# Performance work log

Measured on AMD Instinct MI355X. Metric: run time of the kernel, lower is better.

Reference implementation:

```python
import jax, jax.numpy as jnp
import numpy as np

DIM = 1536      # model dim
NH = 12         # num heads
HD = 128        # head dim
F, H, W = 3, 26, 48   # video latent grid (frames, height, width)
S = F * H * W   # sequence length = 3744
B = 1
EPS = 1e-6
C2 = HD // 2    # 64 rotary pairs per head
SPLITS = [C2 - 2 * (C2 // 3), C2 // 3, C2 // 3]  # [22, 21, 21] for (f, h, w)


def _rope_angles():
    """Wan rope_params: concat of per-axis inverse-frequency angle tables, [1024, 64]."""
    def rp(dim):  # returns [1024, dim//2]
        inv = 1.0 / (10000.0 ** (np.arange(0, dim, 2, dtype=np.float64) / dim))
        return np.outer(np.arange(1024, dtype=np.float64), inv)
    a = np.concatenate([rp(HD - 4 * (HD // 6)), rp(2 * (HD // 6)), rp(2 * (HD // 6))], axis=1)
    return jnp.asarray(a, jnp.float32)


def setup_inputs() -> dict:
    key = jax.random.key(0)
    ks = jax.random.split(key, 9)
    std = DIM ** -0.5
    return {
        "x": jax.random.normal(ks[0], (B, S, DIM), jnp.float32),
        "wq": jax.random.normal(ks[1], (DIM, DIM), jnp.float32) * std,
        "bq": jnp.zeros((DIM,), jnp.float32),
        "wk": jax.random.normal(ks[2], (DIM, DIM), jnp.float32) * std,
        "bk": jnp.zeros((DIM,), jnp.float32),
        "wv": jax.random.normal(ks[3], (DIM, DIM), jnp.float32) * std,
        "bv": jnp.zeros((DIM,), jnp.float32),
        "wo": jax.random.normal(ks[4], (DIM, DIM), jnp.float32) * std,
        "bo": jnp.zeros((DIM,), jnp.float32),
        "gq": jnp.ones((DIM,), jnp.float32),   # WanRMSNorm weight for q
        "gk": jnp.ones((DIM,), jnp.float32),   # WanRMSNorm weight for k
        "freqs": _rope_angles(),                # [1024, 64] rotary angles
        "seq_lens": jnp.full((B,), S, jnp.int32),
    }


def _rmsnorm(y, g):
    return y * jax.lax.rsqrt(jnp.mean(jnp.square(y), axis=-1, keepdims=True) + EPS) * g


def _rope_grid(freqs):
    """Build per-position rotary angles [S, C2] from the 3D grid (F,H,W)."""
    af = freqs[:F, :SPLITS[0]]                       # [F, 22]
    ah = freqs[:H, SPLITS[0]:SPLITS[0] + SPLITS[1]]  # [H, 21]
    aw = freqs[:W, SPLITS[0] + SPLITS[1]:]           # [W, 21]
    ang = jnp.concatenate([
        jnp.broadcast_to(af[:, None, None, :], (F, H, W, SPLITS[0])),
        jnp.broadcast_to(ah[None, :, None, :], (F, H, W, SPLITS[1])),
        jnp.broadcast_to(aw[None, None, :, :], (F, H, W, SPLITS[2])),
    ], axis=-1)
    return ang.reshape(S, C2)


def _rope_apply(t, cos, sin):
    # t: [B, S, NH, HD]; pairs (even, odd) rotated by angle.
    tp = t.reshape(B, S, NH, C2, 2)
    xr, xi = tp[..., 0], tp[..., 1]
    yr = xr * cos - xi * sin
    yi = xr * sin + xi * cos
    return jnp.stack([yr, yi], axis=-1).reshape(B, S, NH, HD)


def reference(x, wq, bq, wk, bk, wv, bv, wo, bo, gq, gk, freqs, seq_lens):
    q = _rmsnorm(x @ wq.T + bq, gq).reshape(B, S, NH, HD)
    k = _rmsnorm(x @ wk.T + bk, gk).reshape(B, S, NH, HD)
    v = (x @ wv.T + bv).reshape(B, S, NH, HD)

    ang = _rope_grid(freqs)                    # [S, C2]
    cos = jnp.cos(ang)[None, :, None, :]       # [1, S, 1, C2]
    sin = jnp.sin(ang)[None, :, None, :]
    q = _rope_apply(q, cos, sin)
    k = _rope_apply(k, cos, sin)

    scale = HD ** -0.5
    scores = jnp.einsum('bqhd,bkhd->bhqk', q, k) * scale   # [B, NH, S, S]
    kmask = jnp.arange(S)[None, :] < seq_lens[:, None]     # [B, S]
    scores = jnp.where(kmask[:, None, None, :], scores, jnp.float32(-1e9))
    attn = jax.nn.softmax(scores, axis=-1)
    out = jnp.einsum('bhqk,bkhd->bqhd', attn, v).reshape(B, S, DIM)
    return out @ wo.T + bo
```

## Files before the change

### kernel.cpp

```cpp
#include <hip/hip_runtime.h>
#include <stdint.h>


#define DIM   1536
#define S_TOT 3744
#define NHEAD 12
#define HD    128
#define QT    59
#define NT    117

using short8 = __attribute__((ext_vector_type(8))) short;
using f32x4  = __attribute__((ext_vector_type(4))) float;
using f32x2  = __attribute__((ext_vector_type(2))) float;

__device__ __forceinline__ unsigned short f2bf(float f) {
  unsigned u = __builtin_bit_cast(unsigned, f);
  u += 0x7fffu + ((u >> 16) & 1u);
  return (unsigned short)(u >> 16);
}

__device__ __forceinline__ void gl_lds16(const void* g, void* l) {
  auto gp = (const __attribute__((address_space(1))) unsigned int*)g;
  auto lp = (__attribute__((address_space(3))) unsigned int*)(uintptr_t)l;
  __builtin_amdgcn_global_load_lds(gp, lp, 16, 0, 0);
}

#define NX4 (S_TOT * DIM / 4)
#define NW4 (DIM * DIM / 4)
__global__ __launch_bounds__(256) void cvt5_kernel(
    const float* __restrict__ x, const float* __restrict__ wq,
    const float* __restrict__ wk, const float* __restrict__ wv,
    const float* __restrict__ wo,
    unsigned short* __restrict__ xb, unsigned short* __restrict__ wqb,
    unsigned short* __restrict__ wkb, unsigned short* __restrict__ wvb,
    unsigned short* __restrict__ wob) {
  int gid = blockIdx.x * 256 + threadIdx.x;
  const float* src; unsigned short* dst; int off;
  if (gid < NX4)                { src = x;  dst = xb;  off = gid; }
  else if (gid < NX4 + NW4)     { src = wq; dst = wqb; off = gid - NX4; }
  else if (gid < NX4 + 2 * NW4) { src = wk; dst = wkb; off = gid - NX4 - NW4; }
  else if (gid < NX4 + 3 * NW4) { src = wv; dst = wvb; off = gid - NX4 - 2 * NW4; }
  else if (gid < NX4 + 4 * NW4) { src = wo; dst = wob; off = gid - NX4 - 3 * NW4; }
  else return;
  float4 v = ((const float4*)src)[off];
  ushort4 o;
  o.x = f2bf(v.x); o.y = f2bf(v.y); o.z = f2bf(v.z); o.w = f2bf(v.w);
  ((ushort4*)dst)[off] = o;
}

__device__ __forceinline__ void gemm_body(const unsigned short* __restrict__ A,
                                          const unsigned short* __restrict__ W,
                                          const float* __restrict__ bias,
                                          float* __restrict__ outF,
                                          unsigned short* __restrict__ outB,
                                          int M, int mode) {
  constexpr int K = DIM, N = DIM;
  __shared__ unsigned short As[128 * 32];
  __shared__ unsigned short Ws[128 * 32];
  int tid = threadIdx.x;
  int w = tid >> 6, lane = tid & 63;
  int wr = w >> 1, wc = w & 1, q4 = lane >> 4, ql = lane & 15;
  int m0 = blockIdx.y * 128, n0 = blockIdx.x * 128;

  f32x4 acc[4][4];
  const f32x4 zero4 = {0.f, 0.f, 0.f, 0.f};
#pragma unroll
  for (int i = 0; i < 4; i++)
#pragma unroll
    for (int j = 0; j < 4; j++) acc[i][j] = zero4;

  for (int k0 = 0; k0 < K; k0 += 32) {
    __syncthreads();
#pragma unroll
    for (int r = 0; r < 2; r++) {
      int idx = r * 256 + tid;
      int row = idx >> 2, ch = idx & 3;
      int am = m0 + row; am = (am < M) ? am : (M - 1);
      gl_lds16(A + (size_t)am * K + k0 + ch * 8, &As[idx * 8]);
      gl_lds16(W + (size_t)(n0 + row) * K + k0 + ch * 8, &Ws[idx * 8]);
    }
    __syncthreads();
    short8 af[4], wf[4];
#pragma unroll
    for (int i = 0; i < 4; i++)
      af[i] = *(const short8*)&As[(wr * 64 + i * 16 + ql) * 32 + q4 * 8];
#pragma unroll
    for (int j = 0; j < 4; j++)
      wf[j] = *(const short8*)&Ws[(wc * 64 + j * 16 + ql) * 32 + q4 * 8];
#pragma unroll
    for (int i = 0; i < 4; i++)
#pragma unroll
      for (int j = 0; j < 4; j++)
        acc[i][j] = __builtin_amdgcn_mfma_f32_16x16x32_bf16(af[i], wf[j], acc[i][j], 0, 0, 0);
  }

  float bb[4];
#pragma unroll
  for (int j = 0; j < 4; j++) bb[j] = bias[n0 + wc * 64 + j * 16 + ql];
#pragma unroll
  for (int i = 0; i < 4; i++) {
#pragma unroll
    for (int rg = 0; rg < 4; rg++) {
      int row = m0 + wr * 64 + i * 16 + q4 * 4 + rg;
      if (row < M) {
#pragma unroll
        for (int j = 0; j < 4; j++) {
          int col = n0 + wc * 64 + j * 16 + ql;
          float v = acc[i][j][rg] + bb[j];
          if (mode == 0) outF[(size_t)row * N + col] = v;
          else           outB[(size_t)row * N + col] = f2bf(v);
        }
      }
    }
  }
}

__global__ __launch_bounds__(256) void gemm_qkv_kernel(
    const unsigned short* __restrict__ xb,
    const unsigned short* __restrict__ wqb, const unsigned short* __restrict__ wkb,
    const unsigned short* __restrict__ wvb,
    const float* __restrict__ bq, const float* __restrict__ bk, const float* __restrict__ bv,
    float* __restrict__ Yq, float* __restrict__ Yk, unsigned short* __restrict__ Vb) {
  int z = blockIdx.z;
  const unsigned short* W = (z == 0) ? wqb : ((z == 1) ? wkb : wvb);
  const float* bias       = (z == 0) ? bq  : ((z == 1) ? bk  : bv);
  float* outF             = (z == 0) ? Yq  : Yk;
  gemm_body(xb, W, bias, outF, Vb, S_TOT, (z == 2) ? 1 : 0);
}

__global__ __launch_bounds__(256) void gemm_out_kernel(
    const unsigned short* __restrict__ AO, const unsigned short* __restrict__ wob,
    const float* __restrict__ bo, float* __restrict__ out) {
  gemm_body(AO, wob, bo, out, nullptr, S_TOT, 0);
}

__global__ __launch_bounds__(256) void normrope_kernel(
    const float* __restrict__ Yq, const float* __restrict__ Yk,
    const float* __restrict__ gq, const float* __restrict__ gk,
    const float* __restrict__ freqs,
    unsigned short* __restrict__ Qb, unsigned short* __restrict__ Kb) {
  int s = blockIdx.x;
  int tid = threadIdx.x;
  int w = tid >> 6, lane = tid & 63;
  const f32x2* yq2 = (const f32x2*)(Yq + (size_t)s * DIM);
  const f32x2* yk2 = (const f32x2*)(Yk + (size_t)s * DIM);
  f32x2 vq[3], vk[3];
  float ssq = 0.f, ssk = 0.f;
#pragma unroll
  for (int r = 0; r < 3; r++) {
    int p = tid + 256 * r;
    vq[r] = yq2[p]; vk[r] = yk2[p];
    ssq += vq[r].x * vq[r].x + vq[r].y * vq[r].y;
    ssk += vk[r].x * vk[r].x + vk[r].y * vk[r].y;
  }
#pragma unroll
  for (int d = 1; d < 64; d <<= 1) {
    ssq += __shfl_xor(ssq, d);
    ssk += __shfl_xor(ssk, d);
  }
  __shared__ float rq[4], rk[4];
  if (lane == 0) { rq[w] = ssq; rk[w] = ssk; }
  __syncthreads();
  float tq = rq[0] + rq[1] + rq[2] + rq[3];
  float tk = rk[0] + rk[1] + rk[2] + rk[3];
  const float SM_L2 = 0.08838834764831845f * 1.4426950408889634f;
  float invq = rsqrtf(tq * (1.f / DIM) + 1e-6f) * SM_L2;
  float invk = rsqrtf(tk * (1.f / DIM) + 1e-6f);

  int fi = s / (26 * 48);
  int hi = (s / 48) % 26;
  int wi = s % 48;
#pragma unroll
  for (int r = 0; r < 3; r++) {
    int p = tid + 256 * r;
    int c = p & 63;
    int frow = (c < 22) ? fi : ((c < 43) ? hi : wi);
    float ang = freqs[frow * 64 + c];
    float sn, cs;
    __sincosf(ang, &sn, &cs);
    {
      float a = vq[r].x * invq * gq[2 * p];
      float b = vq[r].y * invq * gq[2 * p + 1];
      ushort2 o; o.x = f2bf(a * cs - b * sn); o.y = f2bf(a * sn + b * cs);
      ((ushort2*)Qb)[(size_t)s * (DIM / 2) + p] = o;
    }
    {
      float a = vk[r].x * invk * gk[2 * p];
      float b = vk[r].y * invk * gk[2 * p + 1];
      ushort2 o; o.x = f2bf(a * cs - b * sn); o.y = f2bf(a * sn + b * cs);
      ((ushort2*)Kb)[(size_t)s * (DIM / 2) + p] = o;
    }
  }
}

__global__ __launch_bounds__(256) void vtrans_kernel(const unsigned short* __restrict__ Vb,
                                                     unsigned short* __restrict__ Vt) {
  int d0 = blockIdx.x * 64, s0 = blockIdx.y * 64;
  __shared__ unsigned short t[64][65];
  int tid = threadIdx.x;
#pragma unroll
  for (int r = 0; r < 4; r++) {
    int idx = r * 256 + tid;
    int sr = idx >> 4, c4 = (idx & 15) * 4;
    ushort4 v; v.x = v.y = v.z = v.w = 0;
    int s = s0 + sr;
    if (s < S_TOT) v = *(const ushort4*)(Vb + (size_t)s * DIM + d0 + c4);
    t[sr][c4 + 0] = v.x; t[sr][c4 + 1] = v.y; t[sr][c4 + 2] = v.z; t[sr][c4 + 3] = v.w;
  }
  __syncthreads();
#pragma unroll
  for (int r = 0; r < 4; r++) {
    int idx = r * 256 + tid;
    int dr = idx >> 4, s4 = (idx & 15) * 4;
    if (s0 + s4 < S_TOT) {
      ushort4 v;
      v.x = t[s4 + 0][dr]; v.y = t[s4 + 1][dr]; v.z = t[s4 + 2][dr]; v.w = t[s4 + 3][dr];
      *(ushort4*)(Vt + (size_t)(d0 + dr) * S_TOT + s0 + s4) = v;
    }
  }
}

__global__ __launch_bounds__(256, 3) void attn_kernel(
    const unsigned short* __restrict__ Qb, const unsigned short* __restrict__ Kb,
    const unsigned short* __restrict__ Vt, unsigned short* __restrict__ AO,
    const int* __restrict__ seq_lens) {
  const int NWG = QT * NHEAD;
  int bid = blockIdx.x;
  int xcd = bid & 7, bix = bid >> 3;
  const int qc = NWG >> 3, rr = NWG & 7;
  int wg = (xcd < rr ? xcd * (qc + 1) : rr * (qc + 1) + (xcd - rr) * qc) + bix;
  int h  = wg / QT;
  int qt = wg - h * QT;

  int tid = threadIdx.x;
  int w = tid >> 6, lane = tid & 63;
  int q4 = lane >> 4, ql = lane & 15;
  int seqlen = seq_lens[0]; if (seqlen > S_TOT) seqlen = S_TOT;

  __shared__ unsigned short Kl[2][32 * 128];
  __shared__ unsigned short Vl[2][128 * 32];
  __shared__ unsigned short Pl[4][16 * 40];

  int q0 = qt * 64 + w * 16;
  bool wact = (q0 < S_TOT);

  const size_t hoff = (size_t)h * HD;

  auto stage = [&](int buf, int t) {
    int k0 = t * 32;
    const unsigned short* kseg = Kb + (size_t)k0 * DIM + hoff;
#pragma unroll
    for (int r = 0; r < 2; r++) {
      int idx = r * 256 + tid;
      int row = idx >> 4, c = idx & 15;
      int g = c ^ (row & 15);
      gl_lds16(kseg + (size_t)row * DIM + g * 8, &Kl[buf][idx * 8]);
    }
#pragma unroll
    for (int r = 0; r < 2; r++) {
      int idx = r * 256 + tid;
      int row = idx >> 2, c = idx & 3;
      int g = c ^ (row & 3);
      gl_lds16(Vt + (hoff + row) * S_TOT + k0 + g * 8, &Vl[buf][idx * 8]);
    }
  };

  short8 qf[4];
  {
    int qrow = q0 + ql; if (qrow > S_TOT - 1) qrow = S_TOT - 1;
#pragma unroll
    for (int ks = 0; ks < 4; ks++)
      qf[ks] = *(const short8*)(Qb + (size_t)qrow * DIM + hoff + ks * 32 + q4 * 8);
  }
  asm volatile("s_waitcnt vmcnt(0)" ::: "memory");

  f32x4 o[8];
  const f32x4 zero4 = {0.f, 0.f, 0.f, 0.f};
#pragma unroll
  for (int nt = 0; nt < 8; nt++) o[nt] = zero4;
  float m_run = -3.0e38f, l_run = 0.f;

  stage(0, 0);

  for (int t = 0; t < NT; ++t) {
    int cur = t & 1;
    int k0 = t * 32;
    __builtin_amdgcn_s_barrier();
    asm volatile("" ::: "memory");
    if (t + 1 < NT) {
      stage(cur ^ 1, t + 1);
      asm volatile("s_waitcnt vmcnt(4)" ::: "memory");
    } else {
      asm volatile("s_waitcnt vmcnt(0)" ::: "memory");
    }
    __builtin_amdgcn_sched_barrier(0);
    __builtin_amdgcn_s_barrier();
    asm volatile("" ::: "memory");
    if (!wact) continue;

    f32x4 st[2];
    __builtin_amdgcn_s_setprio(1);
#pragma unroll
    for (int mt = 0; mt < 2; mt++) {
      st[mt] = zero4;
#pragma unroll
      for (int ks = 0; ks < 4; ks++) {
        int c = (ks * 4 + q4) ^ ql;
        short8 kf = *(const short8*)&Kl[cur][(mt * 16 + ql) * 128 + c * 8];
        st[mt] = __builtin_amdgcn_mfma_f32_16x16x32_bf16(kf, qf[ks], st[mt], 0, 0, 0);
      }
    }
    __builtin_amdgcn_s_setprio(0);

    float sc[8];
#pragma unroll
    for (int mt = 0; mt < 2; mt++)
#pragma unroll
      for (int rg = 0; rg < 4; rg++)
        sc[mt * 4 + rg] = st[mt][rg];
    if (k0 + 32 > seqlen) {
#pragma unroll
      for (int mt = 0; mt < 2; mt++)
#pragma unroll
        for (int rg = 0; rg < 4; rg++) {
          int key = k0 + mt * 16 + q4 * 4 + rg;
          if (key >= seqlen) sc[mt * 4 + rg] = -3.0e38f;
        }
    }
    float mloc = sc[0];
#pragma unroll
    for (int i = 1; i < 8; i++) mloc = fmaxf(mloc, sc[i]);
    mloc = fmaxf(mloc, __shfl_xor(mloc, 16));
    mloc = fmaxf(mloc, __shfl_xor(mloc, 32));

    if (!__all(mloc <= m_run + 8.0f)) {
      float mnew = fmaxf(m_run, mloc);
      float alpha = exp2f(m_run - mnew);
      m_run = mnew;
      l_run *= alpha;
      float ar[4];
#pragma unroll
      for (int rg = 0; rg < 4; rg++) ar[rg] = __shfl(alpha, q4 * 4 + rg, 16);
#pragma unroll
      for (int nt = 0; nt < 8; nt++)
#pragma unroll
        for (int rg = 0; rg < 4; rg++) o[nt][rg] *= ar[rg];
    }

    float lloc = 0.f;
#pragma unroll
    for (int mt = 0; mt < 2; mt++) {
      float p0 = exp2f(sc[mt * 4 + 0] - m_run);
      float p1 = exp2f(sc[mt * 4 + 1] - m_run);
      float p2 = exp2f(sc[mt * 4 + 2] - m_run);
      float p3 = exp2f(sc[mt * 4 + 3] - m_run);
      lloc += p0 + p1 + p2 + p3;
      unsigned pk0, pk1;
      asm("v_cvt_pk_bf16_f32 %0, %1, %2" : "=v"(pk0) : "v"(p0), "v"(p1));
      asm("v_cvt_pk_bf16_f32 %0, %1, %2" : "=v"(pk1) : "v"(p2), "v"(p3));
      uint2 pw; pw.x = pk0; pw.y = pk1;
      *(uint2*)&Pl[w][ql * 40 + mt * 16 + q4 * 4] = pw;
    }
    lloc += __shfl_xor(lloc, 16);
    lloc += __shfl_xor(lloc, 32);
    l_run += lloc;

    short8 pa = *(const short8*)&Pl[w][ql * 40 + q4 * 8];
    __builtin_amdgcn_s_setprio(1);
#pragma unroll
    for (int nt = 0; nt < 8; nt++) {
      int c = q4 ^ (ql & 3);
      short8 vb = *(const short8*)&Vl[cur][(nt * 16 + ql) * 32 + c * 8];
      o[nt] = __builtin_amdgcn_mfma_f32_16x16x32_bf16(pa, vb, o[nt], 0, 0, 0);
    }
    __builtin_amdgcn_s_setprio(0);
  }

  if (wact) {
    float il = 1.0f / l_run;
    float ilr[4];
#pragma unroll
    for (int rg = 0; rg < 4; rg++) ilr[rg] = __shfl(il, q4 * 4 + rg, 16);
#pragma unroll
    for (int rg = 0; rg < 4; rg++) {
      int row = q0 + q4 * 4 + rg;
      if (row < S_TOT) {
#pragma unroll
        for (int nt = 0; nt < 8; nt++)
          AO[(size_t)row * DIM + hoff + nt * 16 + ql] = f2bf(o[nt][rg] * ilr[rg]);
      }
    }
  }
}

extern "C" void kernel_launch(void* const* d_in, const int* in_sizes, int n_in,
                              void* d_out, int out_size, void* d_ws, size_t ws_size,
                              hipStream_t stream) {
  const float* x    = (const float*)d_in[0];
  const float* wq   = (const float*)d_in[1];
  const float* bq   = (const float*)d_in[2];
  const float* wk   = (const float*)d_in[3];
  const float* bk   = (const float*)d_in[4];
  const float* wv   = (const float*)d_in[5];
  const float* bv   = (const float*)d_in[6];
  const float* wo   = (const float*)d_in[7];
  const float* bo   = (const float*)d_in[8];
  const float* gq   = (const float*)d_in[9];
  const float* gk   = (const float*)d_in[10];
  const float* freqs = (const float*)d_in[11];
  const int*   seq  = (const int*)d_in[12];

  char* ws = (char*)d_ws;
  const size_t SZ_X = (size_t)S_TOT * DIM * 2;
  const size_t SZ_W = (size_t)DIM * DIM * 2;
  const size_t SZ_Y = (size_t)S_TOT * DIM * 4;

  unsigned short* xb  = (unsigned short*)(ws);
  unsigned short* wqb = (unsigned short*)(ws + SZ_X);
  unsigned short* wkb = (unsigned short*)(ws + SZ_X + SZ_W);
  unsigned short* wvb = (unsigned short*)(ws + SZ_X + 2 * SZ_W);
  unsigned short* wob = (unsigned short*)(ws + SZ_X + 3 * SZ_W);
  float*          Yq  = (float*)(ws + SZ_X + 4 * SZ_W);
  float*          Yk  = (float*)(ws + SZ_X + 4 * SZ_W + SZ_Y);
  unsigned short* Vb  = (unsigned short*)(ws + SZ_X + 4 * SZ_W + 2 * SZ_Y);
  unsigned short* Qb  = (unsigned short*)(ws + SZ_X + 4 * SZ_W + 2 * SZ_Y + SZ_X);
  unsigned short* Kb  = (unsigned short*)(ws + SZ_X + 4 * SZ_W + 2 * SZ_Y + 2 * SZ_X);
  unsigned short* Vt  = (unsigned short*)(ws + SZ_X + 4 * SZ_W + 2 * SZ_Y + 3 * SZ_X);
  unsigned short* AO  = (unsigned short*)(ws + SZ_X + 4 * SZ_W + 2 * SZ_Y + 4 * SZ_X);

  int total4 = NX4 + 4 * NW4;
  cvt5_kernel<<<dim3((total4 + 255) / 256), 256, 0, stream>>>(
      x, wq, wk, wv, wo, xb, wqb, wkb, wvb, wob);

  gemm_qkv_kernel<<<dim3(DIM / 128, (S_TOT + 127) / 128, 3), 256, 0, stream>>>(
      xb, wqb, wkb, wvb, bq, bk, bv, Yq, Yk, Vb);

  normrope_kernel<<<dim3(S_TOT), 256, 0, stream>>>(Yq, Yk, gq, gk, freqs, Qb, Kb);

  vtrans_kernel<<<dim3(DIM / 64, (S_TOT + 63) / 64), 256, 0, stream>>>(Vb, Vt);

  attn_kernel<<<dim3(QT * NHEAD), 256, 0, stream>>>(Qb, Kb, Vt, AO, seq);

  gemm_out_kernel<<<dim3(DIM / 128, (S_TOT + 127) / 128), 256, 0, stream>>>(
      AO, wob, bo, (float*)d_out);
}
```

Baseline: 428.5 us.

## Split attention over KV halves with a separate combine kernel; load V directly to registers

The attention kernel splits each (head, query-tile) over two halves of the key range, doubling the workgroup count to 1416, and writes unnormalized fp32 partial outputs plus (max, sum) pairs into reused workspace. A new reduce kernel merges the two halves and writes bf16 output. V tiles are no longer staged through LDS; each lane loads its V fragments straight from global memory into registers. The goal is better occupancy on the 256-CU device and less LDS traffic, at the cost of extra partial-output memory traffic, a separate kernel launch, and uncoalesced strided global V loads.

Measured after the change: 544.7 us. +27.1%, slower.

```diff
diff --git a/kernel.cpp b/kernel.cpp
--- a/kernel.cpp
+++ b/kernel.cpp
@@ -8,6 +8,7 @@
 #define HD    128
 #define QT    59
 #define NT    117
+#define KSPLIT 2
 
 using short8 = __attribute__((ext_vector_type(8))) short;
 using f32x4  = __attribute__((ext_vector_type(4))) float;
@@ -220,17 +221,22 @@
   }
 }
 
-__global__ __launch_bounds__(256, 3) void attn_kernel(
+__global__ __launch_bounds__(256, 4) void attn_kernel(
     const unsigned short* __restrict__ Qb, const unsigned short* __restrict__ Kb,
-    const unsigned short* __restrict__ Vt, unsigned short* __restrict__ AO,
+    const unsigned short* __restrict__ Vt,
+    float* __restrict__ Opart, float2* __restrict__ Ml,
     const int* __restrict__ seq_lens) {
-  const int NWG = QT * NHEAD;
+  const int NWG = QT * NHEAD * KSPLIT;
   int bid = blockIdx.x;
   int xcd = bid & 7, bix = bid >> 3;
-  const int qc = NWG >> 3, rr = NWG & 7;
-  int wg = (xcd < rr ? xcd * (qc + 1) : rr * (qc + 1) + (xcd - rr) * qc) + bix;
-  int h  = wg / QT;
-  int qt = wg - h * QT;
+  const int qc = NWG >> 3;
+  int wg = xcd * qc + bix;
+  int qt  = wg % QT;
+  int rem = wg / QT;
+  int h    = rem >> 1;
+  int sidx = rem & 1;
+  int tbeg = sidx ? 59 : 0;
+  int tend = sidx ? NT : 59;
 
   int tid = threadIdx.x;
   int w = tid >> 6, lane = tid & 63;
@@ -238,7 +244,6 @@
   int seqlen = seq_lens[0]; if (seqlen > S_TOT) seqlen = S_TOT;
 
   __shared__ unsigned short Kl[2][32 * 128];
-  __shared__ unsigned short Vl[2][128 * 32];
   __shared__ unsigned short Pl[4][16 * 40];
 
   int q0 = qt * 64 + w * 16;
@@ -256,13 +261,6 @@
       int g = c ^ (row & 15);
       gl_lds16(kseg + (size_t)row * DIM + g * 8, &Kl[buf][idx * 8]);
     }
-#pragma unroll
-    for (int r = 0; r < 2; r++) {
-      int idx = r * 256 + tid;
-      int row = idx >> 2, c = idx & 3;
-      int g = c ^ (row & 3);
-      gl_lds16(Vt + (hoff + row) * S_TOT + k0 + g * 8, &Vl[buf][idx * 8]);
-    }
   };
 
   short8 qf[4];
@@ -274,22 +272,24 @@
   }
   asm volatile("s_waitcnt vmcnt(0)" ::: "memory");
 
+  const unsigned short* vbase = Vt + (size_t)(hoff + ql) * S_TOT + q4 * 8;
+
   f32x4 o[8];
   const f32x4 zero4 = {0.f, 0.f, 0.f, 0.f};
 #pragma unroll
   for (int nt = 0; nt < 8; nt++) o[nt] = zero4;
   float m_run = -3.0e38f, l_run = 0.f;
 
-  stage(0, 0);
-
-  for (int t = 0; t < NT; ++t) {
-    int cur = t & 1;
+  stage(0, tbeg);
+
+  for (int t = tbeg; t < tend; ++t) {
+    int cur = (t - tbeg) & 1;
     int k0 = t * 32;
     __builtin_amdgcn_s_barrier();
     asm volatile("" ::: "memory");
-    if (t + 1 < NT) {
+    if (t + 1 < tend) {
       stage(cur ^ 1, t + 1);
-      asm volatile("s_waitcnt vmcnt(4)" ::: "memory");
+      asm volatile("s_waitcnt vmcnt(2)" ::: "memory");
     } else {
       asm volatile("s_waitcnt vmcnt(0)" ::: "memory");
     }
@@ -311,6 +311,11 @@
       }
     }
     __builtin_amdgcn_s_setprio(0);
+
+    short8 vbr[8];
+#pragma unroll
+    for (int nt = 0; nt < 8; nt++)
+      vbr[nt] = *(const short8*)(vbase + (size_t)nt * (16 * S_TOT) + k0);
 
     float sc[8];
 #pragma unroll
@@ -368,29 +373,46 @@
     short8 pa = *(const short8*)&Pl[w][ql * 40 + q4 * 8];
     __builtin_amdgcn_s_setprio(1);
 #pragma unroll
-    for (int nt = 0; nt < 8; nt++) {
-      int c = q4 ^ (ql & 3);
-      short8 vb = *(const short8*)&Vl[cur][(nt * 16 + ql) * 32 + c * 8];
-      o[nt] = __builtin_amdgcn_mfma_f32_16x16x32_bf16(pa, vb, o[nt], 0, 0, 0);
-    }
+    for (int nt = 0; nt < 8; nt++)
+      o[nt] = __builtin_amdgcn_mfma_f32_16x16x32_bf16(pa, vbr[nt], o[nt], 0, 0, 0);
     __builtin_amdgcn_s_setprio(0);
   }
 
   if (wact) {
-    float il = 1.0f / l_run;
-    float ilr[4];
-#pragma unroll
-    for (int rg = 0; rg < 4; rg++) ilr[rg] = __shfl(il, q4 * 4 + rg, 16);
+    size_t ob = (((size_t)sidx * NHEAD + h) * QT + qt) * (64 * 128);
 #pragma unroll
     for (int rg = 0; rg < 4; rg++) {
-      int row = q0 + q4 * 4 + rg;
-      if (row < S_TOT) {
-#pragma unroll
-        for (int nt = 0; nt < 8; nt++)
-          AO[(size_t)row * DIM + hoff + nt * 16 + ql] = f2bf(o[nt][rg] * ilr[rg]);
-      }
-    }
-  }
+      int row = w * 16 + q4 * 4 + rg;
+#pragma unroll
+      for (int nt = 0; nt < 8; nt++)
+        Opart[ob + (size_t)row * 128 + nt * 16 + ql] = o[nt][rg];
+    }
+    if (lane < 16) {
+      float2 ml; ml.x = m_run; ml.y = l_run;
+      Ml[((size_t)(sidx * NHEAD + h) * QT + qt) * 64 + w * 16 + lane] = ml;
+    }
+  }
+}
+
+__global__ __launch_bounds__(256) void reduce_kernel(
+    const float* __restrict__ Opart, const float2* __restrict__ Ml,
+    unsigned short* __restrict__ AO) {
+  int flat = blockIdx.x * 256 + threadIdx.x;
+  int d = flat & 127;
+  int r = flat >> 7;
+  int h = r / S_TOT;
+  int q = r - h * S_TOT;
+  int qt = q >> 6, qi = q & 63;
+  size_t ob = (((size_t)h * QT) + qt) * (64 * 128) + (size_t)qi * 128 + d;
+  const size_t so = (size_t)NHEAD * QT * 64 * 128;
+  int mb = (h * QT + qt) * 64 + qi;
+  const int sm = NHEAD * QT * 64;
+  float2 ml0 = Ml[mb], ml1 = Ml[mb + sm];
+  float mm = fmaxf(ml0.x, ml1.x);
+  float w0 = exp2f(ml0.x - mm), w1 = exp2f(ml1.x - mm);
+  float l = w0 * ml0.y + w1 * ml1.y;
+  float v = (w0 * Opart[ob] + w1 * Opart[ob + so]) / l;
+  AO[(size_t)q * DIM + h * HD + d] = f2bf(v);
 }
 
 extern "C" void kernel_launch(void* const* d_in, const int* in_sizes, int n_in,
@@ -415,18 +437,23 @@
   const size_t SZ_W = (size_t)DIM * DIM * 2;
   const size_t SZ_Y = (size_t)S_TOT * DIM * 4;
 
-  unsigned short* xb  = (unsigned short*)(ws);
-  unsigned short* wqb = (unsigned short*)(ws + SZ_X);
-  unsigned short* wkb = (unsigned short*)(ws + SZ_X + SZ_W);
-  unsigned short* wvb = (unsigned short*)(ws + SZ_X + 2 * SZ_W);
-  unsigned short* wob = (unsigned short*)(ws + SZ_X + 3 * SZ_W);
-  float*          Yq  = (float*)(ws + SZ_X + 4 * SZ_W);
-  float*          Yk  = (float*)(ws + SZ_X + 4 * SZ_W + SZ_Y);
-  unsigned short* Vb  = (unsigned short*)(ws + SZ_X + 4 * SZ_W + 2 * SZ_Y);
-  unsigned short* Qb  = (unsigned short*)(ws + SZ_X + 4 * SZ_W + 2 * SZ_Y + SZ_X);
-  unsigned short* Kb  = (unsigned short*)(ws + SZ_X + 4 * SZ_W + 2 * SZ_Y + 2 * SZ_X);
-  unsigned short* Vt  = (unsigned short*)(ws + SZ_X + 4 * SZ_W + 2 * SZ_Y + 3 * SZ_X);
-  unsigned short* AO  = (unsigned short*)(ws + SZ_X + 4 * SZ_W + 2 * SZ_Y + 4 * SZ_X);
+  size_t off = 0;
+  unsigned short* xb  = (unsigned short*)(ws + off); off += SZ_X;
+  unsigned short* wob = (unsigned short*)(ws + off); off += SZ_W;
+  float*          Yq  = (float*)(ws + off);          off += SZ_Y;
+  float*          Yk  = (float*)(ws + off);          off += SZ_Y;
+  unsigned short* wqb = (unsigned short*)(ws + off); off += SZ_W;
+  unsigned short* wkb = (unsigned short*)(ws + off); off += SZ_W;
+  unsigned short* wvb = (unsigned short*)(ws + off); off += SZ_W;
+  unsigned short* Vb  = (unsigned short*)(ws + off); off += SZ_X;
+  unsigned short* Qb  = (unsigned short*)(ws + off); off += SZ_X;
+  unsigned short* Kb  = (unsigned short*)(ws + off); off += SZ_X;
+  unsigned short* Vt  = (unsigned short*)(ws + off); off += SZ_X;
+  unsigned short* AO  = (unsigned short*)(ws + off); off += SZ_X;
+
+  float*  Opart = (float*)Yq;
+  float2* Ml    = (float2*)((char*)Yq +
+                  (size_t)KSPLIT * NHEAD * QT * 64 * 128 * sizeof(float));
 
   int total4 = NX4 + 4 * NW4;
   cvt5_kernel<<<dim3((total4 + 255) / 256), 256, 0, stream>>>(
@@ -439,7 +466,10 @@
 
   vtrans_kernel<<<dim3(DIM / 64, (S_TOT + 63) / 64), 256, 0, stream>>>(Vb, Vt);
 
-  attn_kernel<<<dim3(QT * NHEAD), 256, 0, stream>>>(Qb, Kb, Vt, AO, seq);
+  attn_kernel<<<dim3(QT * NHEAD * KSPLIT), 256, 0, stream>>>(
+      Qb, Kb, Vt, Opart, Ml, seq);
+
+  reduce_kernel<<<dim3(NHEAD * S_TOT * HD / 256), 256, 0, stream>>>(Opart, Ml, AO);
 
   gemm_out_kernel<<<dim3(DIM / 128, (S_TOT + 127) / 128), 256, 0, stream>>>(
       AO, wob, bo, (float*)d_out);
```
